# Optimization experiments

Measured on AMD Instinct MI355X. Metric: run time of the kernel, lower is better.

Reference implementation:

```python
import jax, jax.numpy as jnp
import numpy as np
from jax import lax

B, N, C = 8, 16384, 4
NUM_GROUPS = 128
GROUP_SIZE = 32
GROUP_RADIUS = 0.1
UPSCALE_K = 128
OVERLAP_FACTOR = 0.7


def setup_inputs() -> dict:
    key = jax.random.key(0)
    k1, k2 = jax.random.split(key)
    # xyz in [0,1]^3, energy in [0,1] at channel 3
    points = jax.random.uniform(k1, (B, N, C), dtype=jnp.float32)
    lengths = jax.random.randint(k2, (B,), N // 2, N + 1).astype(jnp.int32)
    return {"points": points, "lengths": lengths}


def _fps(xyz, lengths, K):
    """Farthest point sampling. xyz: (B,N,3) -> centers (B,K,3), idx (B,K)."""
    B_, N_, _ = xyz.shape
    valid = jnp.arange(N_)[None, :] < lengths[:, None]          # (B,N)
    mind0 = jnp.where(valid, jnp.inf, -jnp.inf)                 # running min dist
    start = jnp.zeros((B_,), jnp.int32)                         # fixed start point
    batch = jnp.arange(B_)

    def step(carry, _):
        mind, cur = carry
        c = xyz[batch, cur]                                     # (B,3)
        d = jnp.sum((xyz - c[:, None, :]) ** 2, axis=-1)        # (B,N)
        mind = jnp.minimum(mind, jnp.where(valid, d, -jnp.inf))
        nxt = jnp.argmax(mind, axis=1).astype(jnp.int32)
        return (mind, nxt), cur

    _, idxs = lax.scan(step, (mind0, start), None, length=K)
    idxs = idxs.T                                               # (B,K)
    centers = xyz[batch[:, None], idxs]                         # (B,K,3)
    return centers, idxs


def _cnms(centers, radius, overlap_factor):
    """Greedy cluster-NMS over FPS-ordered centers. Returns keep mask (B,G)."""
    B_, G, _ = centers.shape
    d2 = jnp.sum((centers[:, :, None, :] - centers[:, None, :, :]) ** 2, axis=-1)
    thr = (2.0 * radius * (1.0 - overlap_factor)) ** 2          # spheres overlap > factor

    def step(keep, j):
        conflict = jnp.any(keep & (d2[:, j, :] < thr), axis=-1)
        keep = keep.at[:, j].set(~conflict)
        return keep, None

    keep, _ = lax.scan(step, jnp.zeros((B_, G), bool), jnp.arange(G))
    return keep


def _ball_query(centers, xyz, lengths, retain, K, radius):
    """First-K points within radius of each center (pytorch3d semantics); -1 pad."""
    N_ = xyz.shape[1]
    d2 = jnp.sum((centers[:, :, None, :] - xyz[:, None, :, :]) ** 2, axis=-1)  # (B,G,N)
    in_len = (jnp.arange(N_)[None, :] < lengths[:, None])[:, None, :]
    valid = (d2 <= radius * radius) & in_len & retain[:, :, None]
    # pick the K smallest point indices among valid ones -> "first K found"
    key_ = jnp.where(valid, jnp.arange(N_, dtype=jnp.int32)[None, None, :], N_)
    negv, _ = lax.top_k(-key_, K)                               # (B,G,K)
    idx = -negv
    return jnp.where(idx == N_, -1, idx)


def reference(points, lengths):
    xyz = points[..., :3]
    centers, _ = _fps(xyz, lengths, NUM_GROUPS)                 # (B,G,3)
    retain = _cnms(centers, GROUP_RADIUS, OVERLAP_FACTOR)       # (B,G)
    idx = _ball_query(centers, xyz, lengths, retain, UPSCALE_K, GROUP_RADIUS)

    # select_topk_by_energy (energies_idx = 3)
    batch = jnp.arange(points.shape[0])[:, None, None]
    invalid = idx == -1
    energies = jnp.where(invalid, -jnp.inf, points[batch, jnp.clip(idx, 0), 3])
    topv, topi = lax.top_k(energies, GROUP_SIZE)                # (B,G,K_new)
    tidx = jnp.take_along_axis(idx, topi, axis=2)
    tidx = jnp.where(jnp.isneginf(topv), -1, tidx)

    # fill_empty_indices: replace -1 with the group's first index
    fidx = jnp.where(tidx == -1, tidx[:, :, :1], tidx)

    # masked_gather: -1 -> gather 0 then zero out
    groups = points[batch, jnp.clip(fidx, 0)]                   # (B,G,K,C)
    groups = jnp.where((fidx == -1)[..., None], 0.0, groups)

    group_lengths = jnp.sum(jnp.all(tidx != -1, axis=2), axis=1)  # (B,)
    embedding_mask = jnp.arange(NUM_GROUPS)[None, :] < group_lengths[:, None]

    # center xyz channels, then scale ALL channels by radius (as in source)
    groups = groups.at[..., :3].add(-centers[:, :, None, :])
    groups = groups / GROUP_RADIUS
    return groups, centers, embedding_mask
```

## Files before the change

### kernel.cpp

```cpp
#include <hip/hip_runtime.h>
#include <math.h>

#define B_ 8
#define N_ 16384
#define G_ 128
#define GS_ 32
#define UK_ 128
#define FPS_T 1024
#define FPS_W 16
#define PPT 16
#define BQ_T 512
#define BQ_W 8

__device__ __forceinline__ float dist2(float x, float y, float z,
                                       float cx, float cy, float cz) {
    float dx = __fsub_rn(x, cx);
    float dy = __fsub_rn(y, cy);
    float dz = __fsub_rn(z, cz);
    return __fadd_rn(__fadd_rn(__fmul_rn(dx, dx), __fmul_rn(dy, dy)),
                     __fmul_rn(dz, dz));
}

__device__ __forceinline__ unsigned long long shfl_xor_u64(unsigned long long v, int m) {
    int lo = __shfl_xor((int)(unsigned)(v & 0xffffffffull), m);
    int hi = __shfl_xor((int)(unsigned)(v >> 32), m);
    return ((unsigned long long)(unsigned)hi << 32) | (unsigned)lo;
}

__device__ __forceinline__ unsigned long long umax64(unsigned long long a,
                                                     unsigned long long b) {
    return a > b ? a : b;
}

__device__ __forceinline__ unsigned wave_umax_bcast(unsigned v) {
    unsigned t;
    t = (unsigned)__builtin_amdgcn_update_dpp(0, (int)v, 0x111, 0xf, 0xf, false); v = v > t ? v : t;
    t = (unsigned)__builtin_amdgcn_update_dpp(0, (int)v, 0x112, 0xf, 0xf, false); v = v > t ? v : t;
    t = (unsigned)__builtin_amdgcn_update_dpp(0, (int)v, 0x114, 0xf, 0xf, false); v = v > t ? v : t;
    t = (unsigned)__builtin_amdgcn_update_dpp(0, (int)v, 0x118, 0xf, 0xf, false); v = v > t ? v : t;
    t = (unsigned)__builtin_amdgcn_update_dpp(0, (int)v, 0x142, 0xa, 0xf, false); v = v > t ? v : t;
    t = (unsigned)__builtin_amdgcn_update_dpp(0, (int)v, 0x143, 0xc, 0xf, false); v = v > t ? v : t;
    return (unsigned)__builtin_amdgcn_readlane((int)v, 63);
}
__device__ __forceinline__ unsigned wave_umin_bcast(unsigned v) {
    unsigned t;
    t = (unsigned)__builtin_amdgcn_update_dpp(-1, (int)v, 0x111, 0xf, 0xf, false); v = v < t ? v : t;
    t = (unsigned)__builtin_amdgcn_update_dpp(-1, (int)v, 0x112, 0xf, 0xf, false); v = v < t ? v : t;
    t = (unsigned)__builtin_amdgcn_update_dpp(-1, (int)v, 0x114, 0xf, 0xf, false); v = v < t ? v : t;
    t = (unsigned)__builtin_amdgcn_update_dpp(-1, (int)v, 0x118, 0xf, 0xf, false); v = v < t ? v : t;
    t = (unsigned)__builtin_amdgcn_update_dpp(-1, (int)v, 0x142, 0xa, 0xf, false); v = v < t ? v : t;
    t = (unsigned)__builtin_amdgcn_update_dpp(-1, (int)v, 0x143, 0xc, 0xf, false); v = v < t ? v : t;
    return (unsigned)__builtin_amdgcn_readlane((int)v, 63);
}

__global__ __launch_bounds__(FPS_T, 4) void fps_cnms_kernel(
    const float4* __restrict__ pts, const int* __restrict__ lengths,
    float* __restrict__ centers_out, int* __restrict__ keep_out,
    int* __restrict__ gl) {
    const int b = blockIdx.x;
    const int t = threadIdx.x;
    const int lane = t & 63;
    const int wv = t >> 6;
    const int len = lengths[b];
    const float4* p = pts + (size_t)b * N_;

    __shared__ float4 s_xy4[N_ / 2];
    __shared__ __align__(16) unsigned long long s_part[FPS_W];
    __shared__ int s_bcn[2];
    __shared__ float s_cen[G_][3];

    float zs[PPT], mind[PPT];
#pragma unroll
    for (int i2 = 0; i2 < PPT / 2; i2++) {
        int nA = (2 * i2) * FPS_T + t;
        int nB = (2 * i2 + 1) * FPS_T + t;
        float4 qA = p[nA];
        float4 qB = p[nB];
        s_xy4[i2 * FPS_T + t] = make_float4(qA.x, qA.y, qB.x, qB.y);
        zs[2 * i2]     = qA.z;
        zs[2 * i2 + 1] = qB.z;
        mind[2 * i2]     = (nA < len) ? INFINITY : -INFINITY;
        mind[2 * i2 + 1] = (nB < len) ? INFINITY : -INFINITY;
    }
    __syncthreads();

    int n = 0;
    for (int k = 0; k < G_; k++) {
        float4 c = p[n];
        float cx = c.x, cy = c.y, cz = c.z;
        if (t == 0) {
            centers_out[(b * G_ + k) * 3 + 0] = cx;
            centers_out[(b * G_ + k) * 3 + 1] = cy;
            centers_out[(b * G_ + k) * 3 + 2] = cz;
            s_cen[k][0] = cx; s_cen[k][1] = cy; s_cen[k][2] = cz;
        }
        if (k == G_ - 1) break;

        float bv = -INFINITY;
        int bn = 0x7fffffff;
#pragma unroll
        for (int i2 = 0; i2 < PPT / 2; i2++) {
            float4 xy = s_xy4[i2 * FPS_T + t];
            float dA = dist2(xy.x, xy.y, zs[2 * i2],     cx, cy, cz);
            float dB = dist2(xy.z, xy.w, zs[2 * i2 + 1], cx, cy, cz);
            float mA = fminf(mind[2 * i2], dA);
            float mB = fminf(mind[2 * i2 + 1], dB);
            mind[2 * i2] = mA;
            mind[2 * i2 + 1] = mB;
            if (mA > bv) { bv = mA; bn = (2 * i2) * FPS_T + t; }
            if (mB > bv) { bv = mB; bn = (2 * i2 + 1) * FPS_T + t; }
        }
        unsigned u = __float_as_uint(bv);
        u = (u & 0x80000000u) ? ~u : (u | 0x80000000u);

        unsigned wmax = wave_umax_bcast(u);
        unsigned ik = (u == wmax) ? (unsigned)bn : 0xffffffffu;
        unsigned wbn = wave_umin_bcast(ik);

        if (lane == 0)
            s_part[wv] = ((unsigned long long)wmax << 32) | (unsigned)(~wbn);
        __syncthreads();

        if (wv == 0) {
            unsigned long long kk = s_part[lane & 15];
#pragma unroll
            for (int off = 8; off; off >>= 1)
                kk = umax64(kk, shfl_xor_u64(kk, off));
            if (lane == 0)
                s_bcn[k & 1] = (int)(~(unsigned)(kk & 0xffffffffull));
        }
        __syncthreads();
        n = s_bcn[k & 1];
    }

    if (t == FPS_T - 1) gl[b] = 0;

    if (t < 64) {
        const float THR = (float)((2.0 * 0.1 * (1.0 - 0.7)) * (2.0 * 0.1 * (1.0 - 0.7)));
        float ax = s_cen[t][0],      ay = s_cen[t][1],      az = s_cen[t][2];
        float ex = s_cen[t + 64][0], ey = s_cen[t + 64][1], ez = s_cen[t + 64][2];
        bool k0 = false, k1 = false;
        for (int j = 0; j < G_; j++) {
            float jx = s_cen[j][0], jy = s_cen[j][1], jz = s_cen[j][2];
            bool c0 = k0 && (dist2(ax, ay, az, jx, jy, jz) < THR);
            bool c1 = k1 && (dist2(ex, ey, ez, jx, jy, jz) < THR);
            bool conflict = __any(c0 || c1);
            if (j == t)      k0 = !conflict;
            if (j == t + 64) k1 = !conflict;
        }
        keep_out[b * G_ + t]      = k0 ? 1 : 0;
        keep_out[b * G_ + t + 64] = k1 ? 1 : 0;
    }
}

__global__ __launch_bounds__(BQ_T) void group_kernel(
    const float4* __restrict__ pts, const int* __restrict__ lengths,
    const float* __restrict__ centers, const int* __restrict__ keep,
    float* __restrict__ groups_out, int* __restrict__ gl) {
    const int bid = blockIdx.x;
    const int b = bid >> 7;
    const int t = threadIdx.x;
    const int lane = t & 63;
    const int wv = t >> 6;

    const float cx = centers[bid * 3 + 0];
    const float cy = centers[bid * 3 + 1];
    const float cz = centers[bid * 3 + 2];
    float4* out4 = (float4*)(groups_out + (size_t)bid * GS_ * 4);

    if (!keep[bid]) {
        if (t < GS_) {
            float4 o;
            o.x = __fdiv_rn(__fsub_rn(0.f, cx), 0.1f);
            o.y = __fdiv_rn(__fsub_rn(0.f, cy), 0.1f);
            o.z = __fdiv_rn(__fsub_rn(0.f, cz), 0.1f);
            o.w = 0.f;
            out4[t] = o;
        }
        return;
    }

    __shared__ int   s_widx[BQ_W][UK_];
    __shared__ float s_wen[BQ_W][UK_];
    __shared__ int   s_wcnt[BQ_W];
    __shared__ int   s_list[UK_];
    __shared__ float s_en[UK_];
    __shared__ int   s_ord[GS_];

    const int len = lengths[b];
    const float R2 = (float)(0.1 * 0.1);
    const float4* p = pts + (size_t)b * N_;

    {
        const int base0 = wv * (N_ / BQ_W);
        int cnt = 0;
        for (int it = 0; it < (N_ / BQ_W) / 64; it++) {
            int n = base0 + it * 64 + lane;
            float4 q = p[n];
            float d2 = dist2(q.x, q.y, q.z, cx, cy, cz);
            bool pred = (n < len) && (d2 <= R2);
            unsigned long long m = __ballot(pred);
            int prefix = __popcll(m & ((1ull << lane) - 1ull));
            int slot = cnt + prefix;
            if (pred && slot < UK_) { s_widx[wv][slot] = n; s_wen[wv][slot] = q.w; }
            cnt += __popcll(m);
        }
        if (lane == 0) s_wcnt[wv] = (cnt < UK_) ? cnt : UK_;
    }
    __syncthreads();

    int M = 0;
#pragma unroll
    for (int w = 0; w < BQ_W; w++) M += s_wcnt[w];
    if (M > UK_) M = UK_;

    if (t < UK_ && t < M) {
        int j = t, w = 0;
        while (w < BQ_W - 1 && j >= s_wcnt[w]) { j -= s_wcnt[w]; w++; }
        s_list[t] = s_widx[w][j];
        s_en[t]   = s_wen[w][j];
    }
    __syncthreads();

    if (wv == 0) {
        float v0 = (lane < M) ? s_en[lane] : -INFINITY;
        float v1 = (lane + 64 < M) ? s_en[lane + 64] : -INFINITY;
        for (int k = 0; k < GS_; k++) {
            float bv; int bs;
            if (v0 >= v1) { bv = v0; bs = lane; }
            else          { bv = v1; bs = lane + 64; }
#pragma unroll
            for (int off = 32; off; off >>= 1) {
                float ov = __shfl_xor(bv, off);
                int   os = __shfl_xor(bs, off);
                bool tk = (ov > bv) || (ov == bv && os < bs);
                bv = tk ? ov : bv; bs = tk ? os : bs;
            }
            if (lane == 0) s_ord[k] = (bv == -INFINITY) ? -1 : bs;
            if (bs == lane)           v0 = -INFINITY;
            else if (bs == lane + 64) v1 = -INFINITY;
        }
    }
    __syncthreads();

    if (t < GS_) {
        int o0 = s_ord[0];
        int first = (o0 >= 0) ? s_list[o0] : -1;
        int ok = s_ord[t];
        int ti = (ok >= 0) ? s_list[ok] : -1;
        int f = (ti == -1) ? first : ti;
        float px = 0.f, py = 0.f, pz = 0.f, pw = 0.f;
        if (f >= 0) { float4 q = p[f]; px = q.x; py = q.y; pz = q.z; pw = q.w; }
        float4 o;
        o.x = __fdiv_rn(__fsub_rn(px, cx), 0.1f);
        o.y = __fdiv_rn(__fsub_rn(py, cy), 0.1f);
        o.z = __fdiv_rn(__fsub_rn(pz, cz), 0.1f);
        o.w = __fdiv_rn(pw, 0.1f);
        out4[t] = o;
    }
    if (t == 0 && M >= GS_) atomicAdd(&gl[b], 1);
}

__global__ void mask_kernel(const int* __restrict__ gl, float* __restrict__ mask_out) {
    int t = threadIdx.x;
    int b = t >> 7, g = t & 127;
    mask_out[t] = (g < gl[b]) ? 1.0f : 0.0f;
}

extern "C" void kernel_launch(void* const* d_in, const int* in_sizes, int n_in,
                              void* d_out, int out_size, void* d_ws, size_t ws_size,
                              hipStream_t stream) {
    const float4* pts = (const float4*)d_in[0];
    const int* lengths = (const int*)d_in[1];
    float* out = (float*)d_out;
    float* groups = out;
    float* centers = out + (size_t)B_ * G_ * GS_ * 4;
    float* mask = centers + (size_t)B_ * G_ * 3;
    int* keep = (int*)d_ws;
    int* gl = keep + B_ * G_;

    hipLaunchKernelGGL(fps_cnms_kernel, dim3(B_), dim3(FPS_T), 0, stream,
                       pts, lengths, centers, keep, gl);
    hipLaunchKernelGGL(group_kernel, dim3(B_ * G_), dim3(BQ_T), 0, stream,
                       pts, lengths, centers, keep, groups, gl);
    hipLaunchKernelGGL(mask_kernel, dim3(1), dim3(B_ * G_), 0, stream, gl, mask);
}
```

Baseline: 330.6 us.

## Split FPS across four blocks per batch with global atomic argmax exchange

Farthest point sampling for each batch now runs on four cooperating blocks, each owning a quarter of the points, instead of one block. Every iteration they exchange their per-block best candidate through per-iteration global slots, spin-waiting on acquire loads. A small init kernel zeroes these slots and the group counters. This cuts per-block serial work and uses more CUs, at the cost of a cross-block global-memory handshake on each of the 127 iterations. It relies on all 32 blocks being resident at the same time.

```diff
diff --git a/kernel.cpp b/kernel.cpp
--- a/kernel.cpp
+++ b/kernel.cpp
@@ -8,7 +8,9 @@
 #define UK_ 128
 #define FPS_T 1024
 #define FPS_W 16
-#define PPT 16
+#define FPS_BLK 4
+#define SLICE (N_ / FPS_BLK)
+#define PPT (SLICE / FPS_T)
 #define BQ_T 512
 #define BQ_W 8
 
@@ -53,18 +55,29 @@
     return (unsigned)__builtin_amdgcn_readlane((int)v, 63);
 }
 
+__global__ void init_kernel(unsigned long long* __restrict__ slots,
+                            int* __restrict__ gl) {
+    int t = threadIdx.x;
+#pragma unroll
+    for (int i = 0; i < (B_ * G_ * FPS_BLK) / 1024; i++)
+        slots[i * 1024 + t] = 0ull;
+    if (t < B_) gl[t] = 0;
+}
+
 __global__ __launch_bounds__(FPS_T, 4) void fps_cnms_kernel(
     const float4* __restrict__ pts, const int* __restrict__ lengths,
     float* __restrict__ centers_out, int* __restrict__ keep_out,
-    int* __restrict__ gl) {
-    const int b = blockIdx.x;
+    unsigned long long* __restrict__ slots) {
+    const int b = blockIdx.x & 7;
+    const int slice = blockIdx.x >> 3;
     const int t = threadIdx.x;
     const int lane = t & 63;
     const int wv = t >> 6;
     const int len = lengths[b];
     const float4* p = pts + (size_t)b * N_;
-
-    __shared__ float4 s_xy4[N_ / 2];
+    const int base = slice * SLICE;
+
+    __shared__ float4 s_xy4[SLICE / 2];
     __shared__ __align__(16) unsigned long long s_part[FPS_W];
     __shared__ int s_bcn[2];
     __shared__ float s_cen[G_][3];
@@ -72,8 +85,8 @@
     float zs[PPT], mind[PPT];
 #pragma unroll
     for (int i2 = 0; i2 < PPT / 2; i2++) {
-        int nA = (2 * i2) * FPS_T + t;
-        int nB = (2 * i2 + 1) * FPS_T + t;
+        int nA = base + (2 * i2) * FPS_T + t;
+        int nB = base + (2 * i2 + 1) * FPS_T + t;
         float4 qA = p[nA];
         float4 qB = p[nB];
         s_xy4[i2 * FPS_T + t] = make_float4(qA.x, qA.y, qB.x, qB.y);
@@ -88,7 +101,7 @@
     for (int k = 0; k < G_; k++) {
         float4 c = p[n];
         float cx = c.x, cy = c.y, cz = c.z;
-        if (t == 0) {
+        if (slice == 0 && t == 0) {
             centers_out[(b * G_ + k) * 3 + 0] = cx;
             centers_out[(b * G_ + k) * 3 + 1] = cy;
             centers_out[(b * G_ + k) * 3 + 2] = cz;
@@ -107,8 +120,8 @@
             float mB = fminf(mind[2 * i2 + 1], dB);
             mind[2 * i2] = mA;
             mind[2 * i2 + 1] = mB;
-            if (mA > bv) { bv = mA; bn = (2 * i2) * FPS_T + t; }
-            if (mB > bv) { bv = mB; bn = (2 * i2 + 1) * FPS_T + t; }
+            if (mA > bv) { bv = mA; bn = base + (2 * i2) * FPS_T + t; }
+            if (mB > bv) { bv = mB; bn = base + (2 * i2 + 1) * FPS_T + t; }
         }
         unsigned u = __float_as_uint(bv);
         u = (u & 0x80000000u) ? ~u : (u | 0x80000000u);
@@ -126,16 +139,28 @@
 #pragma unroll
             for (int off = 8; off; off >>= 1)
                 kk = umax64(kk, shfl_xor_u64(kk, off));
-            if (lane == 0)
-                s_bcn[k & 1] = (int)(~(unsigned)(kk & 0xffffffffull));
+            if (lane == 0) {
+                unsigned long long* slot = slots + ((size_t)b * G_ + k) * FPS_BLK;
+                __hip_atomic_store(&slot[slice], kk, __ATOMIC_RELEASE,
+                                   __HIP_MEMORY_SCOPE_AGENT);
+                unsigned long long best = kk;
+#pragma unroll
+                for (int j = 0; j < FPS_BLK; j++) {
+                    if (j == slice) continue;
+                    unsigned long long v;
+                    while ((v = __hip_atomic_load(&slot[j], __ATOMIC_ACQUIRE,
+                                                  __HIP_MEMORY_SCOPE_AGENT)) == 0ull)
+                        __builtin_amdgcn_s_sleep(1);
+                    best = umax64(best, v);
+                }
+                s_bcn[k & 1] = (int)(~(unsigned)(best & 0xffffffffull));
+            }
         }
         __syncthreads();
         n = s_bcn[k & 1];
     }
 
-    if (t == FPS_T - 1) gl[b] = 0;
-
-    if (t < 64) {
+    if (slice == 0 && t < 64) {
         const float THR = (float)((2.0 * 0.1 * (1.0 - 0.7)) * (2.0 * 0.1 * (1.0 - 0.7)));
         float ax = s_cen[t][0],      ay = s_cen[t][1],      az = s_cen[t][2];
         float ex = s_cen[t + 64][0], ey = s_cen[t + 64][1], ez = s_cen[t + 64][2];
@@ -276,11 +301,13 @@
     float* groups = out;
     float* centers = out + (size_t)B_ * G_ * GS_ * 4;
     float* mask = centers + (size_t)B_ * G_ * 3;
-    int* keep = (int*)d_ws;
+    unsigned long long* slots = (unsigned long long*)d_ws;
+    int* keep = (int*)(slots + B_ * G_ * FPS_BLK);
     int* gl = keep + B_ * G_;
 
-    hipLaunchKernelGGL(fps_cnms_kernel, dim3(B_), dim3(FPS_T), 0, stream,
-                       pts, lengths, centers, keep, gl);
+    hipLaunchKernelGGL(init_kernel, dim3(1), dim3(1024), 0, stream, slots, gl);
+    hipLaunchKernelGGL(fps_cnms_kernel, dim3(B_ * FPS_BLK), dim3(FPS_T), 0, stream,
+                       pts, lengths, centers, keep, slots);
     hipLaunchKernelGGL(group_kernel, dim3(B_ * G_), dim3(BQ_T), 0, stream,
                        pts, lengths, centers, keep, groups, gl);
     hipLaunchKernelGGL(mask_kernel, dim3(1), dim3(B_ * G_), 0, stream, gl, mask);
```

Result: slower. 411.8 us (+24.6%).
